# Kernel optimization log

Measured on AMD Instinct MI355X. Metric: run time of the kernel, lower is better.

The kernel has to match this reference:

```python
import jax, jax.numpy as jnp
import numpy as np

U = 200000      # unique nodes
B = 20000       # node_list batch size
K = 33          # n_nbr_samples + self
F = 256         # feature_dim
E = 128         # emb_dim
BN_EPS = 1e-5


def setup_inputs() -> dict:
    key = jax.random.key(0)
    k1, k2, k3, k4 = jax.random.split(key, 4)
    return {
        "features": jax.random.normal(k1, (U, F), dtype=jnp.float32),
        "W": jax.random.normal(k2, (F, E), dtype=jnp.float32) * 0.05,
        "b": jax.random.normal(k3, (E,), dtype=jnp.float32) * 0.01,
        "gamma": jnp.ones((E,), dtype=jnp.float32),
        "beta": jnp.zeros((E,), dtype=jnp.float32),
        "sample_idx": jax.random.randint(k4, (B, K), 0, U, dtype=jnp.int64)
        if jax.config.jax_enable_x64 else jax.random.randint(k4, (B, K), 0, U, dtype=jnp.int32),
    }


def reference(features, W, b, gamma, beta, sample_idx):
    # fc: Linear -> BatchNorm1d (training-mode batch stats) -> Tanh; Dropout in eval (identity)
    h = features @ W + b                       # [U, E]
    mu = jnp.mean(h, axis=0)                   # [E]
    var = jnp.var(h, axis=0)                   # biased var, as torch BN uses for normalization
    h = jnp.tanh(gamma * (h - mu) * jax.lax.rsqrt(var + BN_EPS) + beta)  # [U, E]
    # Row-normalized 0/1 mask matmul == mean over the K distinct sampled unique-node rows
    gathered = h[sample_idx]                   # [B, K, E] irregular gather
    return jnp.mean(gathered, axis=1)          # [B, E]
```

## Files before the change

### kernel.cpp

```cpp
#include <hip/hip_runtime.h>

#define U_NODES 200000
#define B_ROWS  20000
#define K_S     33
#define F_DIM   256
#define E_DIM   128

typedef __bf16 bf16x8 __attribute__((ext_vector_type(8)));
typedef float  f32x4  __attribute__((ext_vector_type(4)));
typedef unsigned short ushortx8 __attribute__((ext_vector_type(8)));

__device__ __forceinline__ unsigned short f2bf(float f) {
    unsigned int u = __builtin_bit_cast(unsigned int, f);
    u += 0x7fffu + ((u >> 16) & 1u);
    return (unsigned short)(u >> 16);
}
__device__ __forceinline__ float bf2f(unsigned short s) {
    return __builtin_bit_cast(float, ((unsigned int)s) << 16);
}

__global__ void wprep_kernel(const float* __restrict__ W, unsigned short* __restrict__ Wt) {
    int n = blockIdx.x;
    int k = threadIdx.x;
    Wt[n * F_DIM + k] = f2bf(W[(size_t)k * E_DIM + n]);
}

__global__ __launch_bounds__(256) void gemm_stats_kernel(
    const float* __restrict__ A, const unsigned short* __restrict__ Wt,
    unsigned short* __restrict__ h, float* __restrict__ gsum, float* __restrict__ gsq)
{
    __shared__ __attribute__((aligned(16))) char smem[32768];

    const int t    = threadIdx.x;
    const int lane = t & 63;
    const int wv   = t >> 6;
    const int m    = lane & 15;
    const int qd   = lane >> 4;
    const int row0 = blockIdx.x * 128;

    const int r0 = row0 + wv * 32 + m;
    const int r1 = r0 + 16;
    const float* A0 = A + (size_t)min(r0, U_NODES - 1) * F_DIM + qd * 8;
    const float* A1 = A + (size_t)min(r1, U_NODES - 1) * F_DIM + qd * 8;

    f32x4 acc0[8], acc1[8];
    #pragma unroll
    for (int ct = 0; ct < 8; ++ct) {
        acc0[ct] = (f32x4){0.f, 0.f, 0.f, 0.f};
        acc1[ct] = (f32x4){0.f, 0.f, 0.f, 0.f};
    }

    #pragma unroll
    for (int half = 0; half < 2; ++half) {
        if (half) __syncthreads();
        #pragma unroll
        for (int i = 0; i < 8; ++i) {
            int of = t + 256 * i;
            int n = of >> 4, o = of & 15;
            ushortx8 v = *(const ushortx8*)(Wt + n * F_DIM + half * 128 + o * 8);
            *(ushortx8*)(smem + n * 256 + (((o & 8) | ((o ^ n) & 7)) << 4)) = v;
        }
        __syncthreads();
        #pragma unroll
        for (int kf = 0; kf < 4; ++kf) {
            const float* a0p = A0 + half * 128 + kf * 32;
            const float* a1p = A1 + half * 128 + kf * 32;
            float a0f[8], a1f[8];
            *(float4*)&a0f[0] = *(const float4*)(a0p);
            *(float4*)&a0f[4] = *(const float4*)(a0p + 4);
            *(float4*)&a1f[0] = *(const float4*)(a1p);
            *(float4*)&a1f[4] = *(const float4*)(a1p + 4);
            ushortx8 u0, u1;
            #pragma unroll
            for (int j = 0; j < 8; ++j) { u0[j] = f2bf(a0f[j]); u1[j] = f2bf(a1f[j]); }
            bf16x8 a0 = __builtin_bit_cast(bf16x8, u0);
            bf16x8 a1 = __builtin_bit_cast(bf16x8, u1);
            int o = kf * 4 + qd;
            #pragma unroll
            for (int ct = 0; ct < 8; ++ct) {
                int n = ct * 16 + m;
                bf16x8 b = *(const bf16x8*)(smem + n * 256 + (((o & 8) | ((o ^ n) & 7)) << 4));
                acc0[ct] = __builtin_amdgcn_mfma_f32_16x16x32_bf16(a0, b, acc0[ct], 0, 0, 0);
                acc1[ct] = __builtin_amdgcn_mfma_f32_16x16x32_bf16(a1, b, acc1[ct], 0, 0, 0);
            }
        }
    }
    __syncthreads();

    const bool full = (row0 + 128) <= U_NODES;
    float s[8], sq[8];
    #pragma unroll
    for (int ct = 0; ct < 8; ++ct) {
        float ss = 0.f, qq = 0.f;
        #pragma unroll
        for (int v = 0; v < 4; ++v) {
            float x0 = acc0[ct][v];
            float x1 = acc1[ct][v];
            if (full || (row0 + wv * 32 + qd * 4 + v) < U_NODES)      { ss += x0; qq += x0 * x0; }
            if (full || (row0 + wv * 32 + 16 + qd * 4 + v) < U_NODES) { ss += x1; qq += x1 * x1; }
        }
        s[ct] = ss; sq[ct] = qq;
    }
    float* red = (float*)smem;
    int rq = wv * 4 + qd;
    #pragma unroll
    for (int ct = 0; ct < 8; ++ct) red[rq * 128 + ct * 16 + m] = s[ct];
    __syncthreads();
    if (t < 128) {
        float tot = 0.f;
        #pragma unroll
        for (int i = 0; i < 16; ++i) tot += red[i * 128 + t];
        atomicAdd(&gsum[t], tot);
    }
    __syncthreads();
    #pragma unroll
    for (int ct = 0; ct < 8; ++ct) red[rq * 128 + ct * 16 + m] = sq[ct];
    __syncthreads();
    if (t < 128) {
        float tot = 0.f;
        #pragma unroll
        for (int i = 0; i < 16; ++i) tot += red[i * 128 + t];
        atomicAdd(&gsq[t], tot);
    }
    __syncthreads();

    unsigned short* tb = (unsigned short*)(smem + wv * 8192);
    #pragma unroll
    for (int ct = 0; ct < 8; ++ct)
        #pragma unroll
        for (int v = 0; v < 4; ++v) {
            tb[(qd * 4 + v) * 128 + ct * 16 + m]      = f2bf(acc0[ct][v]);
            tb[(16 + qd * 4 + v) * 128 + ct * 16 + m] = f2bf(acc1[ct][v]);
        }
    #pragma unroll
    for (int i = 0; i < 8; ++i) {
        int idx = lane + 64 * i;
        int r = idx >> 4, c8 = (idx & 15) * 8;
        int gr = row0 + wv * 32 + r;
        if (gr < U_NODES)
            *(ushortx8*)(h + (size_t)gr * E_DIM + c8) = *(const ushortx8*)(tb + r * 128 + c8);
    }
}

__global__ void finalize_kernel(const float* __restrict__ gsum, const float* __restrict__ gsq,
                                const float* __restrict__ gamma, const float* __restrict__ beta,
                                float* __restrict__ scale, float* __restrict__ shift)
{
    int e = threadIdx.x;
    float mu  = gsum[e] * (1.f / U_NODES);
    float var = gsq[e] * (1.f / U_NODES) - mu * mu;
    float inv = rsqrtf(var + 1e-5f);
    float sc  = gamma[e] * inv;
    scale[e] = sc;
    shift[e] = beta[e] - sc * mu;
}

__global__ __launch_bounds__(256) void act_kernel(
    unsigned short* __restrict__ h,
    const float* __restrict__ scale, const float* __restrict__ shift)
{
    const int t = threadIdx.x;
    const int g = t & 15;
    float scv[8], shv[8];
    *(float4*)&scv[0] = *(const float4*)(scale + g * 8);
    *(float4*)&scv[4] = *(const float4*)(scale + g * 8 + 4);
    *(float4*)&shv[0] = *(const float4*)(shift + g * 8);
    *(float4*)&shv[4] = *(const float4*)(shift + g * 8 + 4);

    const int NCH = U_NODES * 16;
    for (int c = blockIdx.x * 256 + t; c < NCH; c += gridDim.x * 256) {
        ushortx8* p = (ushortx8*)(h + (size_t)c * 8);
        ushortx8 v = *p;
        #pragma unroll
        for (int j = 0; j < 8; ++j) {
            float x  = bf2f(v[j]) * scv[j] + shv[j];
            float tn = 1.f - 2.f * __builtin_amdgcn_rcpf(__expf(2.f * x) + 1.f);
            v[j] = f2bf(tn);
        }
        *p = v;
    }
}

__global__ __launch_bounds__(256, 4) void gather_kernel(
    const unsigned short* __restrict__ h, const int* __restrict__ sidx_g,
    float* __restrict__ out)
{
    __shared__ int sl[16 * K_S];
    const int t  = threadIdx.x;
    const int g  = t & 15;
    const int r  = t >> 4;
    const int b0 = blockIdx.x * 16;
    for (int i = t; i < 16 * K_S; i += 256) sl[i] = sidx_g[(size_t)b0 * K_S + i];
    __syncthreads();

    float acc[8] = {0.f, 0.f, 0.f, 0.f, 0.f, 0.f, 0.f, 0.f};
    #pragma unroll
    for (int k = 0; k < K_S; ++k) {
        int idx = sl[r * K_S + k];
        ushortx8 v = *(const ushortx8*)(h + (size_t)idx * E_DIM + g * 8);
        #pragma unroll
        for (int j = 0; j < 8; ++j) acc[j] += bf2f(v[j]);
    }
    float* op = out + (size_t)(b0 + r) * E_DIM + g * 8;
    *(float4*)(op)     = make_float4(acc[0] * (1.f / K_S), acc[1] * (1.f / K_S),
                                     acc[2] * (1.f / K_S), acc[3] * (1.f / K_S));
    *(float4*)(op + 4) = make_float4(acc[4] * (1.f / K_S), acc[5] * (1.f / K_S),
                                     acc[6] * (1.f / K_S), acc[7] * (1.f / K_S));
}

extern "C" void kernel_launch(void* const* d_in, const int* in_sizes, int n_in,
                              void* d_out, int out_size, void* d_ws, size_t ws_size,
                              hipStream_t stream) {
    const float* features = (const float*)d_in[0];
    const float* W        = (const float*)d_in[1];
    const float* gamma    = (const float*)d_in[3];
    const float* beta     = (const float*)d_in[4];
    const int*   sample   = (const int*)d_in[5];
    float* out = (float*)d_out;

    float* gsum  = (float*)d_ws;
    float* gsq   = gsum + 128;
    float* scale = gsq + 128;
    float* shift = scale + 128;
    unsigned short* Wt = (unsigned short*)(shift + 128);
    unsigned short* h  = Wt + 128 * 256;

    hipMemsetAsync(gsum, 0, 2 * 128 * sizeof(float), stream);
    wprep_kernel<<<128, 256, 0, stream>>>(W, Wt);
    gemm_stats_kernel<<<(U_NODES + 127) / 128, 256, 0, stream>>>(features, Wt, h, gsum, gsq);
    finalize_kernel<<<1, 128, 0, stream>>>(gsum, gsq, gamma, beta, scale, shift);
    act_kernel<<<1024, 256, 0, stream>>>(h, scale, shift);
    gather_kernel<<<B_ROWS / 16, 256, 0, stream>>>(h, sample, out);
}
```

Before: 365.6 us.

## Fuse BN+tanh into gather and spread stats atomics across partial buffers

Removes the separate activation pass over the whole h buffer and applies the batch-norm affine plus tanh on the fly inside the gather kernel. This trades a full read-modify-write of the node embeddings for extra transcendental work on every gathered element, 33 per output row. Batch statistics are now accumulated into 128 partial slots with a single combined reduction, cutting atomic contention and syncs. The finalize kernel then sums the partials.

Result: faster. 355.4 us (-2.8%).

```diff
diff --git a/kernel.cpp b/kernel.cpp
--- a/kernel.cpp
+++ b/kernel.cpp
@@ -5,6 +5,7 @@
 #define K_S     33
 #define F_DIM   256
 #define E_DIM   128
+#define NPART   128
 
 typedef __bf16 bf16x8 __attribute__((ext_vector_type(8)));
 typedef float  f32x4  __attribute__((ext_vector_type(4)));
@@ -27,7 +28,7 @@
 
 __global__ __launch_bounds__(256) void gemm_stats_kernel(
     const float* __restrict__ A, const unsigned short* __restrict__ Wt,
-    unsigned short* __restrict__ h, float* __restrict__ gsum, float* __restrict__ gsq)
+    unsigned short* __restrict__ h, float* __restrict__ part)
 {
     __shared__ __attribute__((aligned(16))) char smem[32768];
 
@@ -104,23 +105,16 @@
     float* red = (float*)smem;
     int rq = wv * 4 + qd;
     #pragma unroll
-    for (int ct = 0; ct < 8; ++ct) red[rq * 128 + ct * 16 + m] = s[ct];
-    __syncthreads();
-    if (t < 128) {
+    for (int ct = 0; ct < 8; ++ct) {
+        red[rq * 256 + ct * 16 + m]       = s[ct];
+        red[rq * 256 + 128 + ct * 16 + m] = sq[ct];
+    }
+    __syncthreads();
+    {
         float tot = 0.f;
         #pragma unroll
-        for (int i = 0; i < 16; ++i) tot += red[i * 128 + t];
-        atomicAdd(&gsum[t], tot);
-    }
-    __syncthreads();
-    #pragma unroll
-    for (int ct = 0; ct < 8; ++ct) red[rq * 128 + ct * 16 + m] = sq[ct];
-    __syncthreads();
-    if (t < 128) {
-        float tot = 0.f;
-        #pragma unroll
-        for (int i = 0; i < 16; ++i) tot += red[i * 128 + t];
-        atomicAdd(&gsq[t], tot);
+        for (int i = 0; i < 16; ++i) tot += red[i * 256 + t];
+        atomicAdd(&part[(blockIdx.x & (NPART - 1)) * 256 + t], tot);
     }
     __syncthreads();
 
@@ -132,6 +126,7 @@
             tb[(qd * 4 + v) * 128 + ct * 16 + m]      = f2bf(acc0[ct][v]);
             tb[(16 + qd * 4 + v) * 128 + ct * 16 + m] = f2bf(acc1[ct][v]);
         }
+    __syncthreads();
     #pragma unroll
     for (int i = 0; i < 8; ++i) {
         int idx = lane + 64 * i;
@@ -142,47 +137,27 @@
     }
 }
 
-__global__ void finalize_kernel(const float* __restrict__ gsum, const float* __restrict__ gsq,
+__global__ void finalize_kernel(const float* __restrict__ part,
                                 const float* __restrict__ gamma, const float* __restrict__ beta,
                                 float* __restrict__ scale, float* __restrict__ shift)
 {
     int e = threadIdx.x;
-    float mu  = gsum[e] * (1.f / U_NODES);
-    float var = gsq[e] * (1.f / U_NODES) - mu * mu;
+    float sum = 0.f, sq = 0.f;
+    for (int p = 0; p < NPART; ++p) {
+        sum += part[p * 256 + e];
+        sq  += part[p * 256 + 128 + e];
+    }
+    float mu  = sum * (1.f / U_NODES);
+    float var = sq * (1.f / U_NODES) - mu * mu;
     float inv = rsqrtf(var + 1e-5f);
     float sc  = gamma[e] * inv;
     scale[e] = sc;
     shift[e] = beta[e] - sc * mu;
 }
 
-__global__ __launch_bounds__(256) void act_kernel(
-    unsigned short* __restrict__ h,
-    const float* __restrict__ scale, const float* __restrict__ shift)
-{
-    const int t = threadIdx.x;
-    const int g = t & 15;
-    float scv[8], shv[8];
-    *(float4*)&scv[0] = *(const float4*)(scale + g * 8);
-    *(float4*)&scv[4] = *(const float4*)(scale + g * 8 + 4);
-    *(float4*)&shv[0] = *(const float4*)(shift + g * 8);
-    *(float4*)&shv[4] = *(const float4*)(shift + g * 8 + 4);
-
-    const int NCH = U_NODES * 16;
-    for (int c = blockIdx.x * 256 + t; c < NCH; c += gridDim.x * 256) {
-        ushortx8* p = (ushortx8*)(h + (size_t)c * 8);
-        ushortx8 v = *p;
-        #pragma unroll
-        for (int j = 0; j < 8; ++j) {
-            float x  = bf2f(v[j]) * scv[j] + shv[j];
-            float tn = 1.f - 2.f * __builtin_amdgcn_rcpf(__expf(2.f * x) + 1.f);
-            v[j] = f2bf(tn);
-        }
-        *p = v;
-    }
-}
-
 __global__ __launch_bounds__(256, 4) void gather_kernel(
     const unsigned short* __restrict__ h, const int* __restrict__ sidx_g,
+    const float* __restrict__ scale, const float* __restrict__ shift,
     float* __restrict__ out)
 {
     __shared__ int sl[16 * K_S];
@@ -191,6 +166,11 @@
     const int r  = t >> 4;
     const int b0 = blockIdx.x * 16;
     for (int i = t; i < 16 * K_S; i += 256) sl[i] = sidx_g[(size_t)b0 * K_S + i];
+    float scv[8], shv[8];
+    *(float4*)&scv[0] = *(const float4*)(scale + g * 8);
+    *(float4*)&scv[4] = *(const float4*)(scale + g * 8 + 4);
+    *(float4*)&shv[0] = *(const float4*)(shift + g * 8);
+    *(float4*)&shv[4] = *(const float4*)(shift + g * 8 + 4);
     __syncthreads();
 
     float acc[8] = {0.f, 0.f, 0.f, 0.f, 0.f, 0.f, 0.f, 0.f};
@@ -199,7 +179,10 @@
         int idx = sl[r * K_S + k];
         ushortx8 v = *(const ushortx8*)(h + (size_t)idx * E_DIM + g * 8);
         #pragma unroll
-        for (int j = 0; j < 8; ++j) acc[j] += bf2f(v[j]);
+        for (int j = 0; j < 8; ++j) {
+            float x = bf2f(v[j]) * scv[j] + shv[j];
+            acc[j] += 1.f - 2.f * __builtin_amdgcn_rcpf(__expf(2.f * x) + 1.f);
+        }
     }
     float* op = out + (size_t)(b0 + r) * E_DIM + g * 8;
     *(float4*)(op)     = make_float4(acc[0] * (1.f / K_S), acc[1] * (1.f / K_S),
@@ -218,17 +201,15 @@
     const int*   sample   = (const int*)d_in[5];
     float* out = (float*)d_out;
 
-    float* gsum  = (float*)d_ws;
-    float* gsq   = gsum + 128;
-    float* scale = gsq + 128;
+    float* part  = (float*)d_ws;
+    float* scale = part + NPART * 256;
     float* shift = scale + 128;
     unsigned short* Wt = (unsigned short*)(shift + 128);
     unsigned short* h  = Wt + 128 * 256;
 
-    hipMemsetAsync(gsum, 0, 2 * 128 * sizeof(float), stream);
+    hipMemsetAsync(part, 0, NPART * 256 * sizeof(float), stream);
     wprep_kernel<<<128, 256, 0, stream>>>(W, Wt);
-    gemm_stats_kernel<<<(U_NODES + 127) / 128, 256, 0, stream>>>(features, Wt, h, gsum, gsq);
-    finalize_kernel<<<1, 128, 0, stream>>>(gsum, gsq, gamma, beta, scale, shift);
-    act_kernel<<<1024, 256, 0, stream>>>(h, scale, shift);
-    gather_kernel<<<B_ROWS / 16, 256, 0, stream>>>(h, sample, out);
-}
+    gemm_stats_kernel<<<(U_NODES + 127) / 128, 256, 0, stream>>>(features, Wt, h, part);
+    finalize_kernel<<<1, 128, 0, stream>>>(part, gamma, beta, scale, shift);
+    gather_kernel<<<B_ROWS / 16, 256, 0, stream>>>(h, sample, scale, shift, out);
+}
```
